# Kernel tuning notes

Hardware: AMD Instinct MI355X
Metric: run time of the kernel (lower is better)

The kernel has to match this reference:

```python
import jax, jax.numpy as jnp
import numpy as np

B, N, FV_IN, FV_OUT, FE_IN, FE_OUT = 32, 128, 128, 128, 128, 128


def setup_inputs() -> dict:
    key = jax.random.key(0)
    ks = jax.random.split(key, 8)
    s = lambda fan_in: 1.0 / np.sqrt(fan_in)
    return {
        "v_in": jax.random.normal(ks[0], (B, N, FV_IN), dtype=jnp.float32),
        "e_in": jax.random.normal(ks[1], (B, N, N, FE_IN), dtype=jnp.float32),
        # e_vert_layer: Linear(vert_f_in, edge_f_out)
        "W_ev": jax.random.uniform(ks[2], (FV_IN, FE_OUT), jnp.float32, -s(FV_IN), s(FV_IN)),
        "b_ev": jax.random.uniform(ks[3], (FE_OUT,), jnp.float32, -s(FV_IN), s(FV_IN)),
        # e_layer: Linear(edge_f_in, edge_f_out)
        "W_e": jax.random.uniform(ks[4], (FE_IN, FE_OUT), jnp.float32, -s(FE_IN), s(FE_IN)),
        "b_e": jax.random.uniform(ks[5], (FE_OUT,), jnp.float32, -s(FE_IN), s(FE_IN)),
        # v_layer: Linear(vert_f_in + edge_f_out, vert_f_out)
        "W_v": jax.random.uniform(ks[6], (FV_IN + FE_OUT, FV_OUT), jnp.float32, -s(FV_IN + FE_OUT), s(FV_IN + FE_OUT)),
        "b_v": jax.random.uniform(ks[7], (FV_OUT,), jnp.float32, -s(FV_IN + FE_OUT), s(FV_IN + FE_OUT)),
    }


def reference(v_in, e_in, W_ev, b_ev, W_e, b_e, W_v, b_v):
    # per-vertex projection to edge feature space: [B, N, FE_OUT]
    e_v = jnp.einsum("bnf,fg->bng", v_in, W_ev) + b_ev
    # outer vertex sum broadcast: [B, N, N, FE_OUT]
    outer_v_sum = e_v[:, None, :, :] + e_v[:, :, None, :]
    # edge projection: [B, N, N, FE_OUT]
    e = jnp.einsum("bmnf,fg->bmng", e_in, W_e) + b_e
    e_out = jax.nn.relu(e + outer_v_sum)
    # sum-aggregate over dim 1 -> per-vertex edge summary [B, N, FE_OUT]
    per_v_e = jnp.sum(e_out, axis=1)
    vert_e_combined = jnp.concatenate([per_v_e, v_in], axis=2)
    v = jnp.einsum("bnf,fg->bng", vert_e_combined, W_v) + b_v
    v_out = jax.nn.relu(v)
    return (v_out, e_out)
```

## Files before the change

kernel.cpp:

```cpp
#include <hip/hip_runtime.h>
#include <cstdint>
#include <cstring>

#define B_ 32
#define N_ 128
#define F_ 128
#define SPLIT_ 4

typedef __attribute__((ext_vector_type(8))) __bf16 bf16x8;
typedef __attribute__((ext_vector_type(4))) float f32x4;

__device__ inline uint16_t f2bf_bits(float f) {
  __bf16 h = (__bf16)f;
  uint16_t u;
  __builtin_memcpy(&u, &h, 2);
  return u;
}

__global__ __launch_bounds__(128) void ev_kernel(const float* __restrict__ v_in,
                                                 const float* __restrict__ W_ev,
                                                 const float* __restrict__ b_ev,
                                                 float* __restrict__ e_v) {
  __shared__ float vr[8][F_];
  const int R0 = blockIdx.x * 8;
  const int tid = threadIdx.x;
#pragma unroll
  for (int i = 0; i < 8; ++i) vr[i][tid] = v_in[(size_t)(R0 + i) * F_ + tid];
  __syncthreads();
  float acc[8];
  const float bb = b_ev[tid];
#pragma unroll
  for (int i = 0; i < 8; ++i) acc[i] = bb;
  for (int f = 0; f < F_; ++f) {
    const float wv = W_ev[f * F_ + tid];
#pragma unroll
    for (int i = 0; i < 8; ++i) acc[i] += vr[i][f] * wv;
  }
#pragma unroll
  for (int i = 0; i < 8; ++i) e_v[(size_t)(R0 + i) * F_ + tid] = acc[i];
}

__global__ void pack_kernel(const float* __restrict__ W_e, uint32_t* __restrict__ wp) {
  const int idx = blockIdx.x * 256 + threadIdx.x;
  const int t = idx >> 6, l = idx & 63;
  const int kt = t >> 3, gt = t & 7;
  const int kbase = kt * 32 + ((l >> 4) << 3);
  const int g = gt * 16 + (l & 15);
#pragma unroll
  for (int p = 0; p < 4; ++p) {
    const uint32_t lo = f2bf_bits(W_e[(kbase + 2 * p) * F_ + g]);
    const uint32_t hi = f2bf_bits(W_e[(kbase + 2 * p + 1) * F_ + g]);
    wp[idx * 4 + p] = lo | (hi << 16);
  }
}

__global__ __launch_bounds__(256, 4) void main_kernel(
    const float* __restrict__ e_in, const float* __restrict__ e_v,
    const float* __restrict__ b_e, const bf16x8* __restrict__ wp,
    float* __restrict__ e_out, float* __restrict__ pve_part) {
  __shared__ bf16x8 wfrag[2048];
  __shared__ float comb[16][132];

  const int tid = threadIdx.x;
  const int w = tid >> 6, l = tid & 63;
  const int bid = blockIdx.x;
  const int s = bid & 3;
  const int nt = (bid >> 2) & 7;
  const int b = bid >> 5;
  const int n0 = nt * 16;
  const int lr = (l >> 4) << 2;
  const int lc = l & 15;

  for (int i = tid; i < 2048; i += 256) wfrag[i] = wp[i];

  for (int i = tid; i < 2048; i += 256) {
    const int r = i >> 7, g = i & 127;
    comb[r][g] = e_v[((size_t)(b * N_ + n0) + r) * F_ + g] + b_e[g];
  }

  f32x4 pve[8];
#pragma unroll
  for (int gt = 0; gt < 8; ++gt) {
    pve[gt][0] = 0.f; pve[gt][1] = 0.f; pve[gt][2] = 0.f; pve[gt][3] = 0.f;
  }

  __syncthreads();

  const float* einb = e_in + (size_t)b * N_ * N_ * F_;
  float* eoutb = e_out + (size_t)b * N_ * N_ * F_;
  const float* evmb = e_v + (size_t)b * N_ * F_;

  for (int it = 0; it < 8; ++it) {
    const int m = s * 32 + it * 4 + w;
    const float* rowp = einb + ((size_t)m * N_ + n0 + lc) * F_ + ((l >> 4) << 3);
    f32x4 fa0[4], fa1[4];
#pragma unroll
    for (int kt = 0; kt < 4; ++kt) {
      fa0[kt] = *reinterpret_cast<const f32x4*>(rowp + kt * 32);
      fa1[kt] = *reinterpret_cast<const f32x4*>(rowp + kt * 32 + 4);
    }
    bf16x8 a[4];
#pragma unroll
    for (int kt = 0; kt < 4; ++kt) {
#pragma unroll
      for (int e = 0; e < 4; ++e) {
        a[kt][e] = (__bf16)fa0[kt][e];
        a[kt][e + 4] = (__bf16)fa1[kt][e];
      }
    }

    f32x4 acc[8];
#pragma unroll
    for (int gt = 0; gt < 8; ++gt) {
      acc[gt][0] = 0.f; acc[gt][1] = 0.f; acc[gt][2] = 0.f; acc[gt][3] = 0.f;
    }
#pragma unroll
    for (int kt = 0; kt < 4; ++kt)
#pragma unroll
      for (int gt = 0; gt < 8; ++gt)
        acc[gt] = __builtin_amdgcn_mfma_f32_16x16x32_bf16(
            wfrag[(kt * 8 + gt) * 64 + l], a[kt], acc[gt], 0, 0, 0);

    const float* evmr = evmb + (size_t)m * F_;
    float* outp = eoutb + ((size_t)m * N_ + n0 + lc) * F_;
#pragma unroll
    for (int gt = 0; gt < 8; ++gt) {
      const f32x4 evm = *reinterpret_cast<const f32x4*>(evmr + gt * 16 + lr);
      const f32x4 evn = *reinterpret_cast<const f32x4*>(&comb[lc][gt * 16 + lr]);
      f32x4 v = acc[gt] + evn + evm;
#pragma unroll
      for (int q = 0; q < 4; ++q) v[q] = fmaxf(v[q], 0.f);
      pve[gt] += v;
      *reinterpret_cast<f32x4*>(outp + gt * 16 + lr) = v;
    }
  }

  __syncthreads();
  for (int t = 0; t < 4; ++t) {
    if (w == t) {
#pragma unroll
      for (int gt = 0; gt < 8; ++gt) {
        f32x4* cp = reinterpret_cast<f32x4*>(&comb[lc][gt * 16 + lr]);
        if (t == 0) *cp = pve[gt];
        else *cp += pve[gt];
      }
    }
    __syncthreads();
  }

  float* pp = pve_part + (((size_t)s * B_ + b) * N_ + n0) * F_;
  for (int i = tid; i < 512; i += 256) {
    const int r = i >> 5, c = (i & 31) << 2;
    reinterpret_cast<f32x4*>(pp)[i] = *reinterpret_cast<f32x4*>(&comb[r][c]);
  }
}

__global__ __launch_bounds__(128) void v_kernel(
    const float* __restrict__ v_in, const float* __restrict__ pve_part,
    const float* __restrict__ W_v, const float* __restrict__ b_v,
    float* __restrict__ v_out) {
  __shared__ float rows[8][256];
  const int R0 = blockIdx.x * 8;
  const int tid = threadIdx.x;
#pragma unroll
  for (int i = 0; i < 8; ++i) {
    const size_t r = R0 + i;
    float acc = 0.f;
#pragma unroll
    for (int s = 0; s < SPLIT_; ++s)
      acc += pve_part[((size_t)s * B_ * N_ + r) * F_ + tid];
    rows[i][tid] = acc;
    rows[i][128 + tid] = v_in[r * F_ + tid];
  }
  __syncthreads();
  float acc[8];
  const float bb = b_v[tid];
#pragma unroll
  for (int i = 0; i < 8; ++i) acc[i] = bb;
  for (int f = 0; f < 256; ++f) {
    const float wv = W_v[f * F_ + tid];
#pragma unroll
    for (int i = 0; i < 8; ++i) acc[i] += rows[i][f] * wv;
  }
#pragma unroll
  for (int i = 0; i < 8; ++i)
    v_out[(size_t)(R0 + i) * F_ + tid] = fmaxf(acc[i], 0.f);
}

extern "C" void kernel_launch(void* const* d_in, const int* in_sizes, int n_in,
                              void* d_out, int out_size, void* d_ws, size_t ws_size,
                              hipStream_t stream) {
  const float* v_in = (const float*)d_in[0];
  const float* e_in = (const float*)d_in[1];
  const float* W_ev = (const float*)d_in[2];
  const float* b_ev = (const float*)d_in[3];
  const float* W_e  = (const float*)d_in[4];
  const float* b_e  = (const float*)d_in[5];
  const float* W_v  = (const float*)d_in[6];
  const float* b_v  = (const float*)d_in[7];

  float* out = (float*)d_out;
  float* v_out = out;
  float* e_out = out + (size_t)B_ * N_ * F_;

  char* ws = (char*)d_ws;
  float* e_v = (float*)ws;
  uint32_t* wpack = (uint32_t*)(ws + (size_t)2097152);
  float* pve_part = (float*)(ws + (size_t)2097152 + 65536);

  ev_kernel<<<(B_ * N_) / 8, 128, 0, stream>>>(v_in, W_ev, b_ev, e_v);
  pack_kernel<<<8, 256, 0, stream>>>(W_e, wpack);
  main_kernel<<<B_ * 8 * SPLIT_, 256, 0, stream>>>(e_in, e_v, b_e,
                                                   (const bf16x8*)wpack,
                                                   e_out, pve_part);
  v_kernel<<<(B_ * N_) / 8, 128, 0, stream>>>(v_in, pve_part, W_v, b_v, v_out);
}
```

Before: 191.6 us.

## Double-buffer e_in tiles via async global-to-LDS loads with register-resident weights

The main kernel now uses 512 threads. It stages e_in rows into a swizzled, double-buffered LDS tile with global_load_lds, so the next tile's load overlaps the current tile's MFMA work. Each wave keeps its slice of the packed W_e fragments and its e_v+b_e terms in registers instead of LDS. Work is split so each wave handles one m row and two output column tiles. This aims to hide global load latency and cut LDS weight traffic, at the cost of a barrier per iteration and more waves per block.

```diff
diff --git a/kernel.cpp b/kernel.cpp
--- a/kernel.cpp
+++ b/kernel.cpp
@@ -15,6 +15,12 @@
   uint16_t u;
   __builtin_memcpy(&u, &h, 2);
   return u;
+}
+
+__device__ inline void gld16(const float* src, float* dst) {
+  __builtin_amdgcn_global_load_lds(
+      (const __attribute__((address_space(1))) unsigned int*)src,
+      (__attribute__((address_space(3))) unsigned int*)dst, 16, 0, 0);
 }
 
 __global__ __launch_bounds__(128) void ev_kernel(const float* __restrict__ v_in,
@@ -54,105 +60,118 @@
   }
 }
 
-__global__ __launch_bounds__(256, 4) void main_kernel(
+__global__ __launch_bounds__(512, 4) void main_kernel(
     const float* __restrict__ e_in, const float* __restrict__ e_v,
     const float* __restrict__ b_e, const bf16x8* __restrict__ wp,
     float* __restrict__ e_out, float* __restrict__ pve_part) {
-  __shared__ bf16x8 wfrag[2048];
-  __shared__ float comb[16][132];
+  __shared__ __align__(16) float buf[2 * 2 * 2048];
 
   const int tid = threadIdx.x;
   const int w = tid >> 6, l = tid & 63;
   const int bid = blockIdx.x;
-  const int s = bid & 3;
-  const int nt = (bid >> 2) & 7;
-  const int b = bid >> 5;
+  const int s = bid & 3, nt = (bid >> 2) & 7, b = bid >> 5;
   const int n0 = nt * 16;
   const int lr = (l >> 4) << 2;
   const int lc = l & 15;
-
-  for (int i = tid; i < 2048; i += 256) wfrag[i] = wp[i];
-
-  for (int i = tid; i < 2048; i += 256) {
-    const int r = i >> 7, g = i & 127;
-    comb[r][g] = e_v[((size_t)(b * N_ + n0) + r) * F_ + g] + b_e[g];
-  }
-
-  f32x4 pve[8];
-#pragma unroll
-  for (int gt = 0; gt < 8; ++gt) {
-    pve[gt][0] = 0.f; pve[gt][1] = 0.f; pve[gt][2] = 0.f; pve[gt][3] = 0.f;
-  }
-
-  __syncthreads();
-
+  const int ml = w & 1;
+  const int gq = w >> 1;
+  const int m0base = s * 32;
+
+  bf16x8 wreg[4][2];
+#pragma unroll
+  for (int kt = 0; kt < 4; ++kt)
+#pragma unroll
+    for (int j = 0; j < 2; ++j)
+      wreg[kt][j] = wp[(kt * 8 + gq * 2 + j) * 64 + l];
+
+  f32x4 evn[2];
+#pragma unroll
+  for (int j = 0; j < 2; ++j) {
+    const int g0 = (gq * 2 + j) * 16 + lr;
+    evn[j] = *reinterpret_cast<const f32x4*>(&e_v[(size_t)(b * N_ + n0 + lc) * F_ + g0]) +
+             *reinterpret_cast<const f32x4*>(&b_e[g0]);
+  }
+
+  f32x4 pve[2];
+#pragma unroll
+  for (int j = 0; j < 2; ++j) { pve[j][0] = 0.f; pve[j][1] = 0.f; pve[j][2] = 0.f; pve[j][3] = 0.f; }
+
+  const int sw = w >> 2;
+  const int ci = l & 31;
+  const int rpar = l >> 5;
   const float* einb = e_in + (size_t)b * N_ * N_ * F_;
-  float* eoutb = e_out + (size_t)b * N_ * N_ * F_;
-  const float* evmb = e_v + (size_t)b * N_ * F_;
-
-  for (int it = 0; it < 8; ++it) {
-    const int m = s * 32 + it * 4 + w;
-    const float* rowp = einb + ((size_t)m * N_ + n0 + lc) * F_ + ((l >> 4) << 3);
-    f32x4 fa0[4], fa1[4];
+
+#define STAGE(pp, it2)                                                        \
+  {                                                                           \
+    const int m_ = m0base + (it2) * 2 + sw;                                   \
+    const float* mb_ = einb + ((size_t)m_ * N_ + n0) * F_;                    \
+    _Pragma("unroll") for (int j_ = 0; j_ < 2; ++j_) {                        \
+      const int cc_ = ((w << 1) | j_) & 7;                                    \
+      const int r_ = (cc_ << 1) | rpar;                                       \
+      const int sc_ = ci ^ (r_ & 7);                                          \
+      gld16(mb_ + r_ * F_ + sc_ * 4, &buf[(pp) * 4096 + sw * 2048 + (cc_ << 8)]); \
+    }                                                                         \
+  }
+
+  STAGE(0, 0);
+
+  const int swz = lc & 7;
+  for (int it = 0; it < 16; ++it) {
+    const int p = it & 1;
+    __syncthreads();
+    if (it < 15) STAGE(p ^ 1, it + 1);
+
+    const int fbase = p * 4096 + ml * 2048 + lc * 128;
+    f32x4 acc[2];
+#pragma unroll
+    for (int j = 0; j < 2; ++j) { acc[j][0] = 0.f; acc[j][1] = 0.f; acc[j][2] = 0.f; acc[j][3] = 0.f; }
+
 #pragma unroll
     for (int kt = 0; kt < 4; ++kt) {
-      fa0[kt] = *reinterpret_cast<const f32x4*>(rowp + kt * 32);
-      fa1[kt] = *reinterpret_cast<const f32x4*>(rowp + kt * 32 + 4);
+      const int cA = kt * 8 + ((l >> 4) << 1);
+      const f32x4 f0 = *reinterpret_cast<const f32x4*>(&buf[fbase + ((cA ^ swz) << 2)]);
+      const f32x4 f1 = *reinterpret_cast<const f32x4*>(&buf[fbase + (((cA + 1) ^ swz) << 2)]);
+      bf16x8 a;
+#pragma unroll
+      for (int e = 0; e < 4; ++e) {
+        a[e] = (__bf16)f0[e];
+        a[e + 4] = (__bf16)f1[e];
+      }
+      acc[0] = __builtin_amdgcn_mfma_f32_16x16x32_bf16(wreg[kt][0], a, acc[0], 0, 0, 0);
+      acc[1] = __builtin_amdgcn_mfma_f32_16x16x32_bf16(wreg[kt][1], a, acc[1], 0, 0, 0);
     }
-    bf16x8 a[4];
-#pragma unroll
-    for (int kt = 0; kt < 4; ++kt) {
-#pragma unroll
-      for (int e = 0; e < 4; ++e) {
-        a[kt][e] = (__bf16)fa0[kt][e];
-        a[kt][e + 4] = (__bf16)fa1[kt][e];
-      }
+
+    const int m = m0base + it * 2 + ml;
+    const float* evm = &e_v[((size_t)b * N_ + m) * F_];
+    float* op = e_out + (((size_t)(b * N_) + m) * N_ + n0 + lc) * F_;
+#pragma unroll
+    for (int j = 0; j < 2; ++j) {
+      const int g0 = (gq * 2 + j) * 16 + lr;
+      f32x4 v = acc[j] + evn[j] + *reinterpret_cast<const f32x4*>(&evm[g0]);
+#pragma unroll
+      for (int q = 0; q < 4; ++q) v[q] = fmaxf(v[q], 0.f);
+      pve[j] += v;
+      *reinterpret_cast<f32x4*>(&op[g0]) = v;
     }
-
-    f32x4 acc[8];
-#pragma unroll
-    for (int gt = 0; gt < 8; ++gt) {
-      acc[gt][0] = 0.f; acc[gt][1] = 0.f; acc[gt][2] = 0.f; acc[gt][3] = 0.f;
+  }
+
+  __syncthreads();
+  const int sbase = gq * 512 + lc * 32;
+  if (ml == 0) {
+#pragma unroll
+    for (int j = 0; j < 2; ++j)
+      *reinterpret_cast<f32x4*>(&buf[sbase + j * 16 + lr]) = pve[j];
+  }
+  __syncthreads();
+  if (ml == 1) {
+    float* pp = pve_part + (((size_t)s * B_ + b) * N_ + n0 + lc) * F_;
+#pragma unroll
+    for (int j = 0; j < 2; ++j) {
+      const f32x4 sum = pve[j] + *reinterpret_cast<const f32x4*>(&buf[sbase + j * 16 + lr]);
+      *reinterpret_cast<f32x4*>(&pp[(gq * 2 + j) * 16 + lr]) = sum;
     }
-#pragma unroll
-    for (int kt = 0; kt < 4; ++kt)
-#pragma unroll
-      for (int gt = 0; gt < 8; ++gt)
-        acc[gt] = __builtin_amdgcn_mfma_f32_16x16x32_bf16(
-            wfrag[(kt * 8 + gt) * 64 + l], a[kt], acc[gt], 0, 0, 0);
-
-    const float* evmr = evmb + (size_t)m * F_;
-    float* outp = eoutb + ((size_t)m * N_ + n0 + lc) * F_;
-#pragma unroll
-    for (int gt = 0; gt < 8; ++gt) {
-      const f32x4 evm = *reinterpret_cast<const f32x4*>(evmr + gt * 16 + lr);
-      const f32x4 evn = *reinterpret_cast<const f32x4*>(&comb[lc][gt * 16 + lr]);
-      f32x4 v = acc[gt] + evn + evm;
-#pragma unroll
-      for (int q = 0; q < 4; ++q) v[q] = fmaxf(v[q], 0.f);
-      pve[gt] += v;
-      *reinterpret_cast<f32x4*>(outp + gt * 16 + lr) = v;
-    }
-  }
-
-  __syncthreads();
-  for (int t = 0; t < 4; ++t) {
-    if (w == t) {
-#pragma unroll
-      for (int gt = 0; gt < 8; ++gt) {
-        f32x4* cp = reinterpret_cast<f32x4*>(&comb[lc][gt * 16 + lr]);
-        if (t == 0) *cp = pve[gt];
-        else *cp += pve[gt];
-      }
-    }
-    __syncthreads();
-  }
-
-  float* pp = pve_part + (((size_t)s * B_ + b) * N_ + n0) * F_;
-  for (int i = tid; i < 512; i += 256) {
-    const int r = i >> 5, c = (i & 31) << 2;
-    reinterpret_cast<f32x4*>(pp)[i] = *reinterpret_cast<f32x4*>(&comb[r][c]);
-  }
+  }
+#undef STAGE
 }
 
 __global__ __launch_bounds__(128) void v_kernel(
@@ -210,7 +229,7 @@
 
   ev_kernel<<<(B_ * N_) / 8, 128, 0, stream>>>(v_in, W_ev, b_ev, e_v);
   pack_kernel<<<8, 256, 0, stream>>>(W_e, wpack);
-  main_kernel<<<B_ * 8 * SPLIT_, 256, 0, stream>>>(e_in, e_v, b_e,
+  main_kernel<<<B_ * 8 * SPLIT_, 512, 0, stream>>>(e_in, e_v, b_e,
                                                    (const bf16x8*)wpack,
                                                    e_out, pve_part);
   v_kernel<<<(B_ * N_) / 8, 128, 0, stream>>>(v_in, pve_part, W_v, b_v, v_out);
```

Measured after the change: 157.9 us. -17.6%, faster.

## Double-buffer e_in tiles into LDS via async global_load_lds with per-wave pipelining

Applied to the files above, without the earlier changes.

The main kernel now uses 128-thread blocks where each wave owns 16 consecutive m rows. It streams e_in tiles into a swizzled double-buffered LDS area with global_load_lds and explicit vmcnt waits, so loads overlap with MFMA work. The W_e fragments are also loaded directly into LDS, and the ev bias is folded into the accumulator init. The cross-wave LDS reduction is dropped by writing per-wave partials (SPLIT_ raised to 8), which trades more partial-sum traffic for fewer syncs. The risks are lower occupancy from launch_bounds(128,1) with a large LDS footprint, and fragile hand-written waitcnt counts.

```diff
diff --git a/kernel.cpp b/kernel.cpp
--- a/kernel.cpp
+++ b/kernel.cpp
@@ -5,7 +5,7 @@
 #define B_ 32
 #define N_ 128
 #define F_ 128
-#define SPLIT_ 4
+#define SPLIT_ 8
 
 typedef __attribute__((ext_vector_type(8))) __bf16 bf16x8;
 typedef __attribute__((ext_vector_type(4))) float f32x4;
@@ -15,6 +15,12 @@
   uint16_t u;
   __builtin_memcpy(&u, &h, 2);
   return u;
+}
+
+__device__ inline void gld16(const float* src, float* dst) {
+  __builtin_amdgcn_global_load_lds(
+      (const __attribute__((address_space(1))) unsigned int*)src,
+      (__attribute__((address_space(3))) unsigned int*)dst, 16, 0, 0);
 }
 
 __global__ __launch_bounds__(128) void ev_kernel(const float* __restrict__ v_in,
@@ -54,29 +60,41 @@
   }
 }
 
-__global__ __launch_bounds__(256, 4) void main_kernel(
+__global__ __launch_bounds__(128, 1) void main_kernel(
     const float* __restrict__ e_in, const float* __restrict__ e_v,
-    const float* __restrict__ b_e, const bf16x8* __restrict__ wp,
+    const float* __restrict__ b_e, const float* __restrict__ wpf,
     float* __restrict__ e_out, float* __restrict__ pve_part) {
-  __shared__ bf16x8 wfrag[2048];
-  __shared__ float comb[16][132];
+  __shared__ __align__(16) float wlds[8192];
+  __shared__ __align__(16) float abuf[2][2][2048];
 
   const int tid = threadIdx.x;
   const int w = tid >> 6, l = tid & 63;
   const int bid = blockIdx.x;
-  const int s = bid & 3;
-  const int nt = (bid >> 2) & 7;
-  const int b = bid >> 5;
+  const int mc = bid & 3, nt = (bid >> 2) & 7, b = bid >> 5;
   const int n0 = nt * 16;
   const int lr = (l >> 4) << 2;
   const int lc = l & 15;
-
-  for (int i = tid; i < 2048; i += 256) wfrag[i] = wp[i];
-
-  for (int i = tid; i < 2048; i += 256) {
-    const int r = i >> 7, g = i & 127;
-    comb[r][g] = e_v[((size_t)(b * N_ + n0) + r) * F_ + g] + b_e[g];
-  }
+  const int m0 = (mc * 2 + w) * 16;
+  const int swz = lc & 7;
+
+  const float* einb = e_in + (size_t)b * N_ * N_ * F_;
+  const float* evb = e_v + (size_t)b * N_ * F_;
+
+  f32x4 evn[8];
+#pragma unroll
+  for (int gt = 0; gt < 8; ++gt) {
+    const int g0 = gt * 16 + lr;
+    evn[gt] = *reinterpret_cast<const f32x4*>(&evb[(size_t)(n0 + lc) * F_ + g0]) +
+              *reinterpret_cast<const f32x4*>(&b_e[g0]);
+  }
+
+#pragma unroll
+  for (int q = 0; q < 16; ++q) {
+    const int idx = w * 16 + q;
+    gld16(wpf + idx * 256 + l * 4, &wlds[idx * 256]);
+  }
+  asm volatile("s_waitcnt vmcnt(0)" ::: "memory");
+  __syncthreads();
 
   f32x4 pve[8];
 #pragma unroll
@@ -84,75 +102,94 @@
     pve[gt][0] = 0.f; pve[gt][1] = 0.f; pve[gt][2] = 0.f; pve[gt][3] = 0.f;
   }
 
-  __syncthreads();
-
-  const float* einb = e_in + (size_t)b * N_ * N_ * F_;
-  float* eoutb = e_out + (size_t)b * N_ * N_ * F_;
-  const float* evmb = e_v + (size_t)b * N_ * F_;
-
-  for (int it = 0; it < 8; ++it) {
-    const int m = s * 32 + it * 4 + w;
-    const float* rowp = einb + ((size_t)m * N_ + n0 + lc) * F_ + ((l >> 4) << 3);
-    f32x4 fa0[4], fa1[4];
+  f32x4 evm[8];
+
+#define STAGE(dst, mm)                                              \
+  {                                                                 \
+    const float* tb_ = einb + ((size_t)(mm) * N_ + n0) * F_;        \
+    _Pragma("unroll") for (int k_ = 0; k_ < 8; ++k_) {              \
+      const int r_ = k_ * 2 + (l >> 5);                             \
+      const int c_ = (l & 31) ^ (r_ & 7);                           \
+      gld16(tb_ + r_ * F_ + c_ * 4, &(dst)[k_ * 256]);              \
+    }                                                               \
+  }
+#define EVML(mm)                                                    \
+  {                                                                 \
+    _Pragma("unroll") for (int gt_ = 0; gt_ < 8; ++gt_) {           \
+      evm[gt_] = *reinterpret_cast<const f32x4*>(                   \
+          &evb[(size_t)(mm) * F_ + gt_ * 16 + lr]);                 \
+    }                                                               \
+  }
+
+  STAGE(abuf[w][0], m0 + 0);
+  EVML(m0 + 0);
+  STAGE(abuf[w][1], m0 + 1);
+
+#pragma unroll
+  for (int it = 0; it < 16; ++it) {
+    if (it == 0 || it == 15) {
+      asm volatile("s_waitcnt vmcnt(8)" ::: "memory");
+    } else {
+      asm volatile("s_waitcnt vmcnt(16)" ::: "memory");
+    }
+    __builtin_amdgcn_sched_barrier(0);
+
+    f32x4 acc[8];
+#pragma unroll
+    for (int gt = 0; gt < 8; ++gt) acc[gt] = evn[gt] + evm[gt];
+    __builtin_amdgcn_sched_barrier(0);
+
+    const float* fb = abuf[w][it & 1];
+    bf16x8 a[4];
 #pragma unroll
     for (int kt = 0; kt < 4; ++kt) {
-      fa0[kt] = *reinterpret_cast<const f32x4*>(rowp + kt * 32);
-      fa1[kt] = *reinterpret_cast<const f32x4*>(rowp + kt * 32 + 4);
-    }
-    bf16x8 a[4];
+      const int cA = kt * 8 + ((l >> 4) << 1);
+      const f32x4 f0 = *reinterpret_cast<const f32x4*>(&fb[lc * 128 + ((cA ^ swz) << 2)]);
+      const f32x4 f1 = *reinterpret_cast<const f32x4*>(&fb[lc * 128 + (((cA + 1) ^ swz) << 2)]);
+#pragma unroll
+      for (int e = 0; e < 4; ++e) {
+        a[kt][e] = (__bf16)f0[e];
+        a[kt][e + 4] = (__bf16)f1[e];
+      }
+    }
+    asm volatile("s_waitcnt lgkmcnt(0)" ::: "memory");
+    __builtin_amdgcn_sched_barrier(0);
+
+    if (it < 15) EVML(m0 + it + 1);
+    if (it < 14) STAGE(abuf[w][it & 1], m0 + it + 2);
+    __builtin_amdgcn_sched_barrier(0);
+
 #pragma unroll
     for (int kt = 0; kt < 4; ++kt) {
 #pragma unroll
-      for (int e = 0; e < 4; ++e) {
-        a[kt][e] = (__bf16)fa0[kt][e];
-        a[kt][e + 4] = (__bf16)fa1[kt][e];
+      for (int gt = 0; gt < 8; ++gt) {
+        const bf16x8 wf = *reinterpret_cast<const bf16x8*>(
+            &wlds[((kt * 8 + gt) * 64 + l) * 4]);
+        acc[gt] = __builtin_amdgcn_mfma_f32_16x16x32_bf16(wf, a[kt], acc[gt], 0, 0, 0);
       }
     }
 
-    f32x4 acc[8];
+    const int m = m0 + it;
+    float* op = e_out + (((size_t)(b * N_) + m) * N_ + n0 + lc) * F_;
 #pragma unroll
     for (int gt = 0; gt < 8; ++gt) {
-      acc[gt][0] = 0.f; acc[gt][1] = 0.f; acc[gt][2] = 0.f; acc[gt][3] = 0.f;
-    }
-#pragma unroll
-    for (int kt = 0; kt < 4; ++kt)
-#pragma unroll
-      for (int gt = 0; gt < 8; ++gt)
-        acc[gt] = __builtin_amdgcn_mfma_f32_16x16x32_bf16(
-            wfrag[(kt * 8 + gt) * 64 + l], a[kt], acc[gt], 0, 0, 0);
-
-    const float* evmr = evmb + (size_t)m * F_;
-    float* outp = eoutb + ((size_t)m * N_ + n0 + lc) * F_;
-#pragma unroll
-    for (int gt = 0; gt < 8; ++gt) {
-      const f32x4 evm = *reinterpret_cast<const f32x4*>(evmr + gt * 16 + lr);
-      const f32x4 evn = *reinterpret_cast<const f32x4*>(&comb[lc][gt * 16 + lr]);
-      f32x4 v = acc[gt] + evn + evm;
+      const int g0 = gt * 16 + lr;
+      f32x4 v = acc[gt];
 #pragma unroll
       for (int q = 0; q < 4; ++q) v[q] = fmaxf(v[q], 0.f);
       pve[gt] += v;
-      *reinterpret_cast<f32x4*>(outp + gt * 16 + lr) = v;
-    }
-  }
-
-  __syncthreads();
-  for (int t = 0; t < 4; ++t) {
-    if (w == t) {
-#pragma unroll
-      for (int gt = 0; gt < 8; ++gt) {
-        f32x4* cp = reinterpret_cast<f32x4*>(&comb[lc][gt * 16 + lr]);
-        if (t == 0) *cp = pve[gt];
-        else *cp += pve[gt];
-      }
-    }
-    __syncthreads();
-  }
-
-  float* pp = pve_part + (((size_t)s * B_ + b) * N_ + n0) * F_;
-  for (int i = tid; i < 512; i += 256) {
-    const int r = i >> 5, c = (i & 31) << 2;
-    reinterpret_cast<f32x4*>(pp)[i] = *reinterpret_cast<f32x4*>(&comb[r][c]);
-  }
+      *reinterpret_cast<f32x4*>(&op[g0]) = v;
+    }
+    __builtin_amdgcn_sched_barrier(0);
+  }
+#undef STAGE
+#undef EVML
+
+  const int c = mc * 2 + w;
+  float* pp = pve_part + (((size_t)c * B_ + b) * N_ + n0 + lc) * F_;
+#pragma unroll
+  for (int gt = 0; gt < 8; ++gt)
+    *reinterpret_cast<f32x4*>(&pp[gt * 16 + lr]) = pve[gt];
 }
 
 __global__ __launch_bounds__(128) void v_kernel(
@@ -210,8 +247,8 @@
 
   ev_kernel<<<(B_ * N_) / 8, 128, 0, stream>>>(v_in, W_ev, b_ev, e_v);
   pack_kernel<<<8, 256, 0, stream>>>(W_e, wpack);
-  main_kernel<<<B_ * 8 * SPLIT_, 256, 0, stream>>>(e_in, e_v, b_e,
-                                                   (const bf16x8*)wpack,
-                                                   e_out, pve_part);
+  main_kernel<<<B_ * 8 * 4, 128, 0, stream>>>(e_in, e_v, b_e,
+                                              (const float*)wpack,
+                                              e_out, pve_part);
   v_kernel<<<(B_ * N_) / 8, 128, 0, stream>>>(v_in, pve_part, W_v, b_v, v_out);
 }
```

New measurement: 199.1 us. 3.9% more time.
